# Optimization experiments

Measured on AMD Instinct MI355X. Metric: run time of the kernel, lower is better.

## Reference

```python
import jax, jax.numpy as jnp
import numpy as np
from jax import lax

NUM_BLOCKS = 3
NUM_LAYERS = 10
NL = NUM_BLOCKS * NUM_LAYERS  # 30 res blocks
RC = 512   # residual channels
GC = 512   # gate channels
SC = 512   # skip channels
KS = 2     # kernel size
CIN = 128  # local-conditioning channels
FRONT = 32 # front conv kernel size
OUT = 2    # gaussian (mean, log_std)
UPS = [16, 16]  # upsample scales, product = 256 hop
SQRT_HALF = 0.7071067811865476


def causal_conv1d(x, w, b, dilation):
    # x: [B,C_in,T], w: [C_out,C_in,K] -> left-pad only == torch pad-both + trim right (causal SAME)
    pad = dilation * (w.shape[-1] - 1)
    y = lax.conv_general_dilated(x, w, window_strides=(1,), padding=[(pad, 0)],
                                 rhs_dilation=(dilation,),
                                 dimension_numbers=('NCH', 'OIH', 'NCH'))
    return y + b[None, :, None]


def pw(x, w, b):
    # 1x1 conv: w [C_out,C_in]
    return jnp.einsum('oi,bit->bot', w, x) + b[None, :, None]


def upsample(c, up_w, up_b):
    # c: [B,CIN,Tm]; torch ConvTranspose2d(1,1,(3,2s),pad=(1,s//2),stride=(1,s)) + LeakyReLU(0.4)
    h = c[:, None]  # [B,1,CIN,Tm]
    for j, s in enumerate(UPS):
        k = up_w[j][:, :, ::-1, ::-1]  # flip kernel: transposed conv as lhs-dilated conv
        pw_ = 2 * s - 1 - s // 2       # = K - 1 - torch_pad along width
        h = lax.conv_general_dilated(h, k, window_strides=(1, 1),
                                     padding=[(1, 1), (pw_, pw_)],
                                     lhs_dilation=(1, s),
                                     dimension_numbers=('NCHW', 'OIHW', 'NCHW')) + up_b[j]
        h = jnp.where(h > 0, h, 0.4 * h)  # LeakyReLU(0.4)
    return h[:, 0]  # [B,CIN,T]


def setup_inputs() -> dict:
    key = jax.random.key(0)
    ks = iter(jax.random.split(key, 32))
    def rn(shape, scale):
        return jax.random.normal(next(ks), shape, dtype=jnp.float32) * scale
    B, T_mel = 1, 16
    T = T_mel * 256
    return {
        'x': rn((B, 1, T), 1.0),
        'c': rn((B, CIN, T_mel), 1.0),
        'front_w': rn((RC, 1, FRONT), 0.2),
        'front_b': rn((RC,), 0.05),
        'filt_w': rn((NL, GC, RC, KS), 0.03),
        'filt_b': rn((NL, GC), 0.05),
        'gate_w': rn((NL, GC, RC, KS), 0.03),
        'gate_b': rn((NL, GC), 0.05),
        'cf_w': rn((NL, GC, CIN), 0.05),
        'cf_b': rn((NL, GC), 0.05),
        'cg_w': rn((NL, GC, CIN), 0.05),
        'cg_b': rn((NL, GC), 0.05),
        'res_w': rn((NL, RC, GC), 0.04),
        'res_b': rn((NL, RC), 0.05),
        'skip_w': rn((NL, SC, GC), 0.04),
        'skip_b': rn((NL, SC), 0.05),
        'fin1_w': rn((SC, SC), 0.04),
        'fin1_b': rn((SC,), 0.05),
        'fin2_w': rn((OUT, SC), 0.04),
        'fin2_b': rn((OUT,), 0.05),
        'up_w': rn((2, 1, 1, 3, 2 * 16), 0.1),
        'up_b': rn((2,), 0.05),
    }


def reference(x, c, front_w, front_b, filt_w, filt_b, gate_w, gate_b,
              cf_w, cf_b, cg_w, cg_b, res_w, res_b, skip_w, skip_b,
              fin1_w, fin1_b, fin2_w, fin2_b, up_w, up_b):
    c_up = upsample(c, up_w, up_b)                       # [B,CIN,T]
    h = jax.nn.relu(causal_conv1d(x, front_w, front_b, 1))  # [B,RC,T]
    skip = jnp.zeros((x.shape[0], SC, x.shape[2]), x.dtype)
    for i in range(NL):
        d = KS ** (i % NUM_LAYERS)
        f = causal_conv1d(h, filt_w[i], filt_b[i], d) + pw(c_up, cf_w[i], cf_b[i])
        g = causal_conv1d(h, gate_w[i], gate_b[i], d) + pw(c_up, cg_w[i], cg_b[i])
        o = jnp.tanh(f) * jax.nn.sigmoid(g)
        h = (h + pw(o, res_w[i], res_b[i])) * SQRT_HALF
        skip = skip + pw(o, skip_w[i], skip_b[i])
    out = jax.nn.relu(skip)
    out = jax.nn.relu(pw(out, fin1_w, fin1_b))
    return pw(out, fin2_w, fin2_b)  # [B,OUT,T]
```

## Files before the change

### kernel.cpp

```cpp
#include <hip/hip_runtime.h>
#include <hip/hip_bf16.h>

#define TLEN 4096
#define HPADT 512
#define SQRT_HALF 0.70710678118654752f

typedef __attribute__((ext_vector_type(8))) short short8;
typedef __attribute__((ext_vector_type(4))) float floatx4;
typedef __attribute__((ext_vector_type(4))) unsigned short ushort4v;

#define MFMA_BF16(a, b, c) __builtin_amdgcn_mfma_f32_16x16x32_bf16((a), (b), (c), 0, 0, 0)

__device__ __forceinline__ float bf2f(unsigned short u) {
  union { unsigned int i; float f; } v; v.i = ((unsigned int)u) << 16; return v.f;
}
__device__ __forceinline__ unsigned short f2bf(float x) {
  union { float f; unsigned int i; } v; v.f = x;
  unsigned int r = v.i + 0x7FFFu + ((v.i >> 16) & 1u);
  return (unsigned short)(r >> 16);
}
__device__ __forceinline__ short8 ld8(const unsigned short* p) { return *(const short8*)p; }

template <int NI>
__device__ __forceinline__ void stage128(unsigned short* lds, const unsigned short* src,
                                         int stride, int tid) {
  #pragma unroll
  for (int inst = 0; inst < NI; ++inst) {
    int qb = inst * 256 + (tid & 192);
    int q = qb + (tid & 63);
    int r = q >> 4;
    int c = (q & 15) ^ (r & 15);
    __builtin_amdgcn_global_load_lds(
        (const __attribute__((address_space(1))) unsigned int*)(src + (size_t)r * stride + (c << 3)),
        (__attribute__((address_space(3))) unsigned int*)(lds + qb * 8),
        16, 0, 0);
  }
}
__device__ __forceinline__ short8 frag128(const unsigned short* lds, int r, int cj) {
  return *(const short8*)(lds + r * 128 + ((cj ^ (r & 15)) << 3));
}

template <int NI>
__device__ __forceinline__ void stage64(unsigned short* lds, const unsigned short* src,
                                        int stride, int tid) {
  #pragma unroll
  for (int inst = 0; inst < NI; ++inst) {
    int qb = inst * 256 + (tid & 192);
    int q = qb + (tid & 63);
    int r = q >> 3;
    int c = (q & 7) ^ (r & 7);
    __builtin_amdgcn_global_load_lds(
        (const __attribute__((address_space(1))) unsigned int*)(src + (size_t)r * stride + (c << 3)),
        (__attribute__((address_space(3))) unsigned int*)(lds + qb * 8),
        16, 0, 0);
  }
}
__device__ __forceinline__ short8 frag64(const unsigned short* lds, int r, int cj) {
  return *(const short8*)(lds + r * 64 + ((cj ^ (r & 7)) << 3));
}

__device__ __forceinline__ void wait_vm12() { asm volatile("s_waitcnt vmcnt(12)" ::: "memory"); }
__device__ __forceinline__ void wait_vm6()  { asm volatile("s_waitcnt vmcnt(6)"  ::: "memory"); }
__device__ __forceinline__ void wait_vm0()  { asm volatile("s_waitcnt vmcnt(0)"  ::: "memory"); }

__global__ __launch_bounds__(256) void cast_wa_kernel(
    const float* __restrict__ fw, const float* __restrict__ gw,
    unsigned short* __restrict__ WA, int base, int count)
{
  for (int i = blockIdx.x * 256 + threadIdx.x; i < count; i += gridDim.x * 256) {
    size_t idx = (size_t)base + i;
    size_t l = idx >> 16;
    int o = (int)((idx >> 7) & 511);
    int i4 = (int)(idx & 127) * 4;
    const float4* fp = (const float4*)(fw + (((l * 512 + o) * 512 + i4) * 2));
    const float4* gp = (const float4*)(gw + (((l * 512 + o) * 512 + i4) * 2));
    float4 f0 = fp[0], f1v = fp[1];
    float4 g0 = gp[0], g1 = gp[1];
    size_t base0 = ((l * 2 + 0) * 1024);
    size_t base1 = ((l * 2 + 1) * 1024);
    *(ushort4v*)&WA[(base0 + o) * 512 + i4]       = (ushort4v){f2bf(f0.x), f2bf(f0.z), f2bf(f1v.x), f2bf(f1v.z)};
    *(ushort4v*)&WA[(base1 + o) * 512 + i4]       = (ushort4v){f2bf(f0.y), f2bf(f0.w), f2bf(f1v.y), f2bf(f1v.w)};
    *(ushort4v*)&WA[(base0 + 512 + o) * 512 + i4] = (ushort4v){f2bf(g0.x), f2bf(g0.z), f2bf(g1.x), f2bf(g1.z)};
    *(ushort4v*)&WA[(base1 + 512 + o) * 512 + i4] = (ushort4v){f2bf(g0.y), f2bf(g0.w), f2bf(g1.y), f2bf(g1.w)};
  }
}

__global__ __launch_bounds__(256) void cast_rs_kernel(
    const float* __restrict__ rw, const float* __restrict__ sw,
    unsigned short* __restrict__ RS, int base, int count)
{
  for (int i = blockIdx.x * 256 + threadIdx.x; i < count; i += gridDim.x * 256) {
    size_t idx = (size_t)base + i;
    size_t l = idx >> 16;
    int o = (int)((idx >> 7) & 511);
    int i4 = (int)(idx & 127) * 4;
    float4 r4 = *(const float4*)(rw + ((l * 512 + o) * 512 + i4));
    float4 s4 = *(const float4*)(sw + ((l * 512 + o) * 512 + i4));
    *(ushort4v*)&RS[(l * 1024 + o) * 512 + i4]       = (ushort4v){f2bf(r4.x), f2bf(r4.y), f2bf(r4.z), f2bf(r4.w)};
    *(ushort4v*)&RS[(l * 1024 + 512 + o) * 512 + i4] = (ushort4v){f2bf(s4.x), f2bf(s4.y), f2bf(s4.z), f2bf(s4.w)};
  }
}

__global__ __launch_bounds__(256) void cast_misc_kernel(
    const float* __restrict__ cf, const float* __restrict__ cg,
    const float* __restrict__ f1, const float* __restrict__ fb,
    const float* __restrict__ cfb, const float* __restrict__ gb,
    const float* __restrict__ cgb,
    unsigned short* __restrict__ CA, unsigned short* __restrict__ F1c,
    float* __restrict__ fgb)
{
  const int total = 491520 + 65536 + 30720;
  for (int i = blockIdx.x * 256 + threadIdx.x; i < total; i += gridDim.x * 256) {
    if (i < 491520) {
      size_t idx = i;
      size_t l = idx >> 14;
      int o = (int)((idx >> 5) & 511);
      int i4 = (int)(idx & 31) * 4;
      float4 f4 = *(const float4*)(cf + ((l * 512 + o) * 128 + i4));
      float4 g4 = *(const float4*)(cg + ((l * 512 + o) * 128 + i4));
      *(ushort4v*)&CA[(l * 1024 + o) * 128 + i4]       = (ushort4v){f2bf(f4.x), f2bf(f4.y), f2bf(f4.z), f2bf(f4.w)};
      *(ushort4v*)&CA[(l * 1024 + 512 + o) * 128 + i4] = (ushort4v){f2bf(g4.x), f2bf(g4.y), f2bf(g4.z), f2bf(g4.w)};
    } else if (i < 491520 + 65536) {
      size_t idx = i - 491520;
      float4 v = *(const float4*)(f1 + idx * 4);
      *(ushort4v*)&F1c[idx * 4] = (ushort4v){f2bf(v.x), f2bf(v.y), f2bf(v.z), f2bf(v.w)};
    } else {
      int idx = i - (491520 + 65536);
      int l = idx >> 10, r = idx & 1023;
      float v;
      if (r < 512) v = fb[l * 512 + r] + cfb[l * 512 + r];
      else         v = gb[l * 512 + r - 512] + cgb[l * 512 + r - 512];
      fgb[idx] = v;
    }
  }
}


__global__ __launch_bounds__(256) void upsample1_kernel(
    const float* __restrict__ c, const float* __restrict__ up_w,
    const float* __restrict__ up_b, float* __restrict__ u1)
{
  int x = threadIdx.x;
  int h = blockIdx.x;
  const float* w = up_w;
  float acc = 0.f;
  int k1 = (23 - x) & 15;
  #pragma unroll
  for (int dk = 0; dk < 2; ++dk) {
    int kx = k1 + 16 * dk;
    int num = x + kx - 23;
    if (num >= 0) {
      int qq = num >> 4;
      if (qq < 16) {
        #pragma unroll
        for (int ky = 0; ky < 3; ++ky) {
          int hh = h + ky - 1;
          if (hh >= 0 && hh < 128)
            acc += c[hh * 16 + qq] * w[(2 - ky) * 32 + (31 - kx)];
        }
      }
    }
  }
  acc += up_b[0];
  u1[h * 256 + x] = acc > 0.f ? acc : 0.4f * acc;
}

__global__ __launch_bounds__(256) void upsample2_kernel(
    const float* __restrict__ u1, const float* __restrict__ up_w,
    const float* __restrict__ up_b, unsigned short* __restrict__ cu)
{
  int x = blockIdx.x * 256 + threadIdx.x;
  int h = blockIdx.y;
  const float* w = up_w + 96;
  float acc = 0.f;
  int k1 = (23 - x) & 15;
  #pragma unroll
  for (int dk = 0; dk < 2; ++dk) {
    int kx = k1 + 16 * dk;
    int num = x + kx - 23;
    if (num >= 0) {
      int qq = num >> 4;
      if (qq < 256) {
        #pragma unroll
        for (int ky = 0; ky < 3; ++ky) {
          int hh = h + ky - 1;
          if (hh >= 0 && hh < 128)
            acc += u1[hh * 256 + qq] * w[(2 - ky) * 32 + (31 - kx)];
        }
      }
    }
  }
  acc += up_b[1];
  acc = acc > 0.f ? acc : 0.4f * acc;
  cu[(size_t)x * 128 + h] = f2bf(acc);
}

__global__ __launch_bounds__(256) void front_kernel(
    const float* __restrict__ x, const float* __restrict__ fw, const float* __restrict__ fb,
    float* __restrict__ hf, unsigned short* __restrict__ hbf)
{
  __shared__ float xs[40];
  int tid = threadIdx.x;
  int o = blockIdx.y * 256 + tid;
  int t0 = blockIdx.x * 8;
  if (tid < 39) {
    int gx = t0 - 31 + tid;
    xs[tid] = (gx >= 0) ? x[gx] : 0.f;
  }
  __syncthreads();
  float w[32];
  #pragma unroll
  for (int k = 0; k < 32; ++k) w[k] = fw[o * 32 + k];
  float b = fb[o];
  #pragma unroll
  for (int j = 0; j < 8; ++j) {
    float acc = b;
    #pragma unroll
    for (int k = 0; k < 32; ++k) acc += w[k] * xs[j + k];
    acc = acc > 0.f ? acc : 0.f;
    int t = t0 + j;
    hf[(size_t)t * 512 + o] = acc;
    hbf[(size_t)(HPADT + t) * 512 + o] = f2bf(acc);
  }
}

template <int XU>
__global__ __launch_bounds__(256, 2) void gemm_a_smalld_kernel(
    const unsigned short* __restrict__ WA,
    const unsigned short* __restrict__ CA,
    const float* __restrict__ fgb,
    const unsigned short* __restrict__ hbf,
    const unsigned short* __restrict__ cu,
    unsigned short* __restrict__ obf,
    const int d)
{
  __shared__ unsigned short U[2][XU * 32 * 64];
  __shared__ unsigned short Aw[2][4][32 * 64];

  const int tid = threadIdx.x;
  const int lane = tid & 63;
  const int wave = tid >> 6;
  const int lm = lane & 15, qd = lane >> 4;
  const int n0 = blockIdx.x * 128;
  const int m0 = blockIdx.y * 32;
  const int wn = wave * 32;
  const int NS = 10;

  floatx4 accF[2][2], accG[2][2];
  #pragma unroll
  for (int a = 0; a < 2; ++a)
    #pragma unroll
    for (int b = 0; b < 2; ++b) {
      accF[a][b] = (floatx4){0.f, 0.f, 0.f, 0.f};
      accG[a][b] = (floatx4){0.f, 0.f, 0.f, 0.f};
    }

  auto stage_step = [&](int s, int b) {
    if (s < 8) {
      int k0 = s * 64;
      stage64<XU>(&U[b][0], hbf + (size_t)(HPADT + n0 - d) * 512 + k0, 512, tid);
      stage64<1>(&Aw[b][0][0], WA + (size_t)m0 * 512 + k0, 512, tid);
      stage64<1>(&Aw[b][1][0], WA + 524288 + (size_t)m0 * 512 + k0, 512, tid);
      stage64<1>(&Aw[b][2][0], WA + (size_t)(512 + m0) * 512 + k0, 512, tid);
      stage64<1>(&Aw[b][3][0], WA + 524288 + (size_t)(512 + m0) * 512 + k0, 512, tid);
    } else {
      int k0 = (s - 8) * 64;
      stage64<4>(&U[b][0], cu + (size_t)n0 * 128 + k0, 128, tid);
      stage64<1>(&Aw[b][0][0], CA + (size_t)m0 * 128 + k0, 128, tid);
      stage64<1>(&Aw[b][2][0], CA + (size_t)(512 + m0) * 128 + k0, 128, tid);
    }
  };

  stage_step(0, 0);
  #pragma unroll 1
  for (int s = 0; s < NS; ++s) {
    __syncthreads();
    if (s + 1 < NS) stage_step(s + 1, (s + 1) & 1);
    const unsigned short* u   = &U[s & 1][0];
    const unsigned short* af0 = &Aw[s & 1][0][0];
    const unsigned short* af1 = &Aw[s & 1][1][0];
    const unsigned short* ag0 = &Aw[s & 1][2][0];
    const unsigned short* ag1 = &Aw[s & 1][3][0];
    if (s < 8) {
      #pragma unroll
      for (int j = 0; j < 2; ++j) {
        int cj = j * 4 + qd;
        short8 f0a = frag64(af0, lm, cj),      f0b = frag64(af0, 16 + lm, cj);
        short8 f1a = frag64(af1, lm, cj),      f1b = frag64(af1, 16 + lm, cj);
        short8 g0a = frag64(ag0, lm, cj),      g0b = frag64(ag0, 16 + lm, cj);
        short8 g1a = frag64(ag1, lm, cj),      g1b = frag64(ag1, 16 + lm, cj);
        short8 x0 = frag64(u, wn + lm, cj);
        short8 x1 = frag64(u, wn + 16 + lm, cj);
        short8 y0 = frag64(u, d + wn + lm, cj);
        short8 y1 = frag64(u, d + wn + 16 + lm, cj);
        accF[0][0] = MFMA_BF16(f0a, x0, accF[0][0]);
        accF[0][0] = MFMA_BF16(f1a, y0, accF[0][0]);
        accF[0][1] = MFMA_BF16(f0a, x1, accF[0][1]);
        accF[0][1] = MFMA_BF16(f1a, y1, accF[0][1]);
        accF[1][0] = MFMA_BF16(f0b, x0, accF[1][0]);
        accF[1][0] = MFMA_BF16(f1b, y0, accF[1][0]);
        accF[1][1] = MFMA_BF16(f0b, x1, accF[1][1]);
        accF[1][1] = MFMA_BF16(f1b, y1, accF[1][1]);
        accG[0][0] = MFMA_BF16(g0a, x0, accG[0][0]);
        accG[0][0] = MFMA_BF16(g1a, y0, accG[0][0]);
        accG[0][1] = MFMA_BF16(g0a, x1, accG[0][1]);
        accG[0][1] = MFMA_BF16(g1a, y1, accG[0][1]);
        accG[1][0] = MFMA_BF16(g0b, x0, accG[1][0]);
        accG[1][0] = MFMA_BF16(g1b, y0, accG[1][0]);
        accG[1][1] = MFMA_BF16(g0b, x1, accG[1][1]);
        accG[1][1] = MFMA_BF16(g1b, y1, accG[1][1]);
      }
    } else {
      #pragma unroll
      for (int j = 0; j < 2; ++j) {
        int cj = j * 4 + qd;
        short8 fa = frag64(af0, lm, cj), fbv = frag64(af0, 16 + lm, cj);
        short8 ga = frag64(ag0, lm, cj), gbv = frag64(ag0, 16 + lm, cj);
        short8 x0 = frag64(u, wn + lm, cj);
        short8 x1 = frag64(u, wn + 16 + lm, cj);
        accF[0][0] = MFMA_BF16(fa, x0, accF[0][0]);
        accF[0][1] = MFMA_BF16(fa, x1, accF[0][1]);
        accF[1][0] = MFMA_BF16(fbv, x0, accF[1][0]);
        accF[1][1] = MFMA_BF16(fbv, x1, accF[1][1]);
        accG[0][0] = MFMA_BF16(ga, x0, accG[0][0]);
        accG[0][1] = MFMA_BF16(ga, x1, accG[0][1]);
        accG[1][0] = MFMA_BF16(gbv, x0, accG[1][0]);
        accG[1][1] = MFMA_BF16(gbv, x1, accG[1][1]);
      }
    }
  }

  #pragma unroll
  for (int mt = 0; mt < 2; ++mt) {
    int oc0 = m0 + mt * 16 + qd * 4;
    floatx4 fb4 = *(const floatx4*)&fgb[oc0];
    floatx4 gb4 = *(const floatx4*)&fgb[512 + oc0];
    #pragma unroll
    for (int nt = 0; nt < 2; ++nt) {
      int t = n0 + wn + nt * 16 + lm;
      ushort4v o4;
      #pragma unroll
      for (int r = 0; r < 4; ++r) {
        float f = accF[mt][nt][r] + fb4[r];
        float g = accG[mt][nt][r] + gb4[r];
        float ef = __expf(-2.f * f);
        float th = (1.f - ef) / (1.f + ef);
        float sg = 1.f / (1.f + __expf(-g));
        o4[r] = f2bf(th * sg);
      }
      *(ushort4v*)&obf[(size_t)t * 512 + oc0] = o4;
    }
  }
}

__global__ __launch_bounds__(256, 2) void gemm_a_kernel(
    const unsigned short* __restrict__ WA,
    const unsigned short* __restrict__ CA,
    const float* __restrict__ fgb,
    const unsigned short* __restrict__ hbf,
    const unsigned short* __restrict__ cu,
    unsigned short* __restrict__ obf,
    const int d)
{
  __shared__ unsigned short Af[3][32 * 64];
  __shared__ unsigned short Ag[3][32 * 64];
  __shared__ unsigned short Xs[3][128 * 64];

  const int tid = threadIdx.x;
  const int lane = tid & 63;
  const int wave = tid >> 6;
  const int lm = lane & 15, qd = lane >> 4;
  const int n0 = blockIdx.x * 128;
  const int m0 = blockIdx.y * 32;
  const int wn = wave * 32;
  const int NS = 18;

  floatx4 accF[2][2], accG[2][2];
  #pragma unroll
  for (int a = 0; a < 2; ++a)
    #pragma unroll
    for (int b = 0; b < 2; ++b) {
      accF[a][b] = (floatx4){0.f, 0.f, 0.f, 0.f};
      accG[a][b] = (floatx4){0.f, 0.f, 0.f, 0.f};
    }

  auto stage_step = [&](int s, int b) {
    if (s < 16) {
      int tap = s >> 3;
      int k0 = (s & 7) * 64;
      const unsigned short* ab = WA + (size_t)tap * 524288;
      stage64<1>(&Af[b][0], ab + (size_t)m0 * 512 + k0, 512, tid);
      stage64<1>(&Ag[b][0], ab + (size_t)(512 + m0) * 512 + k0, 512, tid);
      stage64<4>(&Xs[b][0], hbf + (size_t)(HPADT + n0 - (tap ? 0 : d)) * 512 + k0, 512, tid);
    } else {
      int k0 = (s - 16) * 64;
      stage64<1>(&Af[b][0], CA + (size_t)m0 * 128 + k0, 128, tid);
      stage64<1>(&Ag[b][0], CA + (size_t)(512 + m0) * 128 + k0, 128, tid);
      stage64<4>(&Xs[b][0], cu + (size_t)n0 * 128 + k0, 128, tid);
    }
  };

  stage_step(0, 0);
  stage_step(1, 1);
  int cur = 0;
  #pragma unroll 1
  for (int s = 0; s < NS; ++s) {
    int stg = cur + 2; if (stg >= 3) stg -= 3;
    if (s + 2 < NS) stage_step(s + 2, stg);
    if (s + 2 < NS)      wait_vm12();
    else if (s + 1 < NS) wait_vm6();
    else                 wait_vm0();
    __builtin_amdgcn_s_barrier();
    __builtin_amdgcn_sched_barrier(0);
    const unsigned short* af = &Af[cur][0];
    const unsigned short* ag = &Ag[cur][0];
    const unsigned short* xs = &Xs[cur][0];
    __builtin_amdgcn_s_setprio(1);
    #pragma unroll
    for (int j = 0; j < 2; ++j) {
      int cj = j * 4 + qd;
      short8 a0 = frag64(af, lm, cj);
      short8 a1 = frag64(af, 16 + lm, cj);
      short8 g0 = frag64(ag, lm, cj);
      short8 g1 = frag64(ag, 16 + lm, cj);
      short8 x0 = frag64(xs, wn + lm, cj);
      short8 x1 = frag64(xs, wn + 16 + lm, cj);
      accF[0][0] = MFMA_BF16(a0, x0, accF[0][0]);
      accF[0][1] = MFMA_BF16(a0, x1, accF[0][1]);
      accF[1][0] = MFMA_BF16(a1, x0, accF[1][0]);
      accF[1][1] = MFMA_BF16(a1, x1, accF[1][1]);
      accG[0][0] = MFMA_BF16(g0, x0, accG[0][0]);
      accG[0][1] = MFMA_BF16(g0, x1, accG[0][1]);
      accG[1][0] = MFMA_BF16(g1, x0, accG[1][0]);
      accG[1][1] = MFMA_BF16(g1, x1, accG[1][1]);
    }
    __builtin_amdgcn_s_setprio(0);
    __builtin_amdgcn_sched_barrier(0);
    __builtin_amdgcn_s_barrier();
    __builtin_amdgcn_sched_barrier(0);
    cur = (cur == 2) ? 0 : cur + 1;
  }

  #pragma unroll
  for (int mt = 0; mt < 2; ++mt) {
    int oc0 = m0 + mt * 16 + qd * 4;
    floatx4 fb4 = *(const floatx4*)&fgb[oc0];
    floatx4 gb4 = *(const floatx4*)&fgb[512 + oc0];
    #pragma unroll
    for (int nt = 0; nt < 2; ++nt) {
      int t = n0 + wn + nt * 16 + lm;
      ushort4v o4;
      #pragma unroll
      for (int r = 0; r < 4; ++r) {
        float f = accF[mt][nt][r] + fb4[r];
        float g = accG[mt][nt][r] + gb4[r];
        float ef = __expf(-2.f * f);
        float th = (1.f - ef) / (1.f + ef);
        float sg = 1.f / (1.f + __expf(-g));
        o4[r] = f2bf(th * sg);
      }
      *(ushort4v*)&obf[(size_t)t * 512 + oc0] = o4;
    }
  }
}

__global__ __launch_bounds__(256, 2) void gemm_b_kernel(
    const unsigned short* __restrict__ RS,
    const float* __restrict__ rb, const float* __restrict__ sb,
    const unsigned short* __restrict__ obf,
    float* __restrict__ hf, unsigned short* __restrict__ hbf,
    float* __restrict__ skip, unsigned short* __restrict__ skipbf,
    const int first, const int last)
{
  __shared__ unsigned short Ar[3][32 * 64];
  __shared__ unsigned short As_[3][32 * 64];
  __shared__ unsigned short Xs[3][128 * 64];

  const int tid = threadIdx.x;
  const int lane = tid & 63;
  const int wave = tid >> 6;
  const int lm = lane & 15, qd = lane >> 4;
  const int n0 = blockIdx.x * 128;
  const int m0 = blockIdx.y * 32;
  const int wn = wave * 32;
  const int NS = 8;

  floatx4 accR[2][2], accS[2][2];
  #pragma unroll
  for (int a = 0; a < 2; ++a)
    #pragma unroll
    for (int b = 0; b < 2; ++b) {
      accR[a][b] = (floatx4){0.f, 0.f, 0.f, 0.f};
      accS[a][b] = (floatx4){0.f, 0.f, 0.f, 0.f};
    }

  auto stage_step = [&](int s, int b) {
    int k0 = s * 64;
    stage64<1>(&Ar[b][0], RS + (size_t)m0 * 512 + k0, 512, tid);
    stage64<1>(&As_[b][0], RS + (size_t)(512 + m0) * 512 + k0, 512, tid);
    stage64<4>(&Xs[b][0], obf + (size_t)n0 * 512 + k0, 512, tid);
  };

  stage_step(0, 0);
  stage_step(1, 1);
  int cur = 0;
  #pragma unroll 1
  for (int s = 0; s < NS; ++s) {
    int stg = cur + 2; if (stg >= 3) stg -= 3;
    if (s + 2 < NS) stage_step(s + 2, stg);
    if (s + 2 < NS)      wait_vm12();
    else if (s + 1 < NS) wait_vm6();
    else                 wait_vm0();
    __builtin_amdgcn_s_barrier();
    __builtin_amdgcn_sched_barrier(0);
    const unsigned short* ar = &Ar[cur][0];
    const unsigned short* as = &As_[cur][0];
    const unsigned short* xs = &Xs[cur][0];
    __builtin_amdgcn_s_setprio(1);
    #pragma unroll
    for (int j = 0; j < 2; ++j) {
      int cj = j * 4 + qd;
      short8 a0 = frag64(ar, lm, cj);
      short8 a1 = frag64(ar, 16 + lm, cj);
      short8 g0 = frag64(as, lm, cj);
      short8 g1 = frag64(as, 16 + lm, cj);
      short8 x0 = frag64(xs, wn + lm, cj);
      short8 x1 = frag64(xs, wn + 16 + lm, cj);
      accR[0][0] = MFMA_BF16(a0, x0, accR[0][0]);
      accR[0][1] = MFMA_BF16(a0, x1, accR[0][1]);
      accR[1][0] = MFMA_BF16(a1, x0, accR[1][0]);
      accR[1][1] = MFMA_BF16(a1, x1, accR[1][1]);
      accS[0][0] = MFMA_BF16(g0, x0, accS[0][0]);
      accS[0][1] = MFMA_BF16(g0, x1, accS[0][1]);
      accS[1][0] = MFMA_BF16(g1, x0, accS[1][0]);
      accS[1][1] = MFMA_BF16(g1, x1, accS[1][1]);
    }
    __builtin_amdgcn_s_setprio(0);
    __builtin_amdgcn_sched_barrier(0);
    __builtin_amdgcn_s_barrier();
    __builtin_amdgcn_sched_barrier(0);
    cur = (cur == 2) ? 0 : cur + 1;
  }

  #pragma unroll
  for (int mt = 0; mt < 2; ++mt) {
    int oc0 = m0 + mt * 16 + qd * 4;
    floatx4 rb4 = *(const floatx4*)&rb[oc0];
    floatx4 sb4 = *(const floatx4*)&sb[oc0];
    #pragma unroll
    for (int nt = 0; nt < 2; ++nt) {
      int t = n0 + wn + nt * 16 + lm;
      size_t base = (size_t)t * 512 + oc0;
      floatx4 h4 = *(const floatx4*)&hf[base];
      floatx4 s4;
      if (first) s4 = (floatx4){0.f, 0.f, 0.f, 0.f};
      else s4 = *(const floatx4*)&skip[base];
      ushort4v hb4;
      #pragma unroll
      for (int r = 0; r < 4; ++r) {
        float hv = (h4[r] + accR[mt][nt][r] + rb4[r]) * SQRT_HALF;
        h4[r] = hv;
        hb4[r] = f2bf(hv);
        s4[r] = s4[r] + accS[mt][nt][r] + sb4[r];
      }
      *(floatx4*)&hf[base] = h4;
      *(ushort4v*)&hbf[(size_t)(HPADT + t) * 512 + oc0] = hb4;
      *(floatx4*)&skip[base] = s4;
      if (last) {
        ushort4v sk4;
        #pragma unroll
        for (int r = 0; r < 4; ++r) sk4[r] = f2bf(s4[r] > 0.f ? s4[r] : 0.f);
        *(ushort4v*)&skipbf[base] = sk4;
      }
    }
  }
}

__global__ __launch_bounds__(256) void final1_kernel(
    const unsigned short* __restrict__ W1,
    const float* __restrict__ b1,
    const unsigned short* __restrict__ skipbf,
    unsigned short* __restrict__ t1)
{
  __shared__ unsigned short Aw[2][64 * 128];
  __shared__ unsigned short Xs[2][128 * 128];

  const int tid = threadIdx.x;
  const int lane = tid & 63;
  const int wave = tid >> 6;
  const int lm = lane & 15, qd = lane >> 4;
  const int n0 = blockIdx.x * 128;
  const int m0 = blockIdx.y * 64;
  const int wm = (wave & 1) * 32;
  const int wn = (wave >> 1) * 64;

  floatx4 acc[2][4];
  #pragma unroll
  for (int a = 0; a < 2; ++a)
    #pragma unroll
    for (int b = 0; b < 4; ++b) acc[a][b] = (floatx4){0.f, 0.f, 0.f, 0.f};

  auto stage_step = [&](int s, int b) {
    int k0 = s * 128;
    stage128<4>(&Aw[b][0], W1 + (size_t)m0 * 512 + k0, 512, tid);
    stage128<8>(&Xs[b][0], skipbf + (size_t)n0 * 512 + k0, 512, tid);
  };

  stage_step(0, 0);
  for (int s = 0; s < 4; ++s) {
    __syncthreads();
    if (s < 3) stage_step(s + 1, (s + 1) & 1);
    const unsigned short* aw = &Aw[s & 1][0];
    const unsigned short* xs = &Xs[s & 1][0];
    #pragma unroll
    for (int j = 0; j < 4; ++j) {
      int cj = j * 4 + qd;
      short8 a[2], xv[4];
      a[0] = frag128(aw, wm + lm, cj);
      a[1] = frag128(aw, wm + 16 + lm, cj);
      #pragma unroll
      for (int nt = 0; nt < 4; ++nt) xv[nt] = frag128(xs, wn + nt * 16 + lm, cj);
      #pragma unroll
      for (int mt = 0; mt < 2; ++mt)
        #pragma unroll
        for (int nt = 0; nt < 4; ++nt)
          acc[mt][nt] = MFMA_BF16(a[mt], xv[nt], acc[mt][nt]);
    }
  }

  #pragma unroll
  for (int mt = 0; mt < 2; ++mt) {
    int oc0 = m0 + wm + mt * 16 + qd * 4;
    floatx4 b4 = *(const floatx4*)&b1[oc0];
    #pragma unroll
    for (int nt = 0; nt < 4; ++nt) {
      int t = n0 + wn + nt * 16 + lm;
      ushort4v o4;
      #pragma unroll
      for (int r = 0; r < 4; ++r) {
        float v = acc[mt][nt][r] + b4[r];
        o4[r] = f2bf(v > 0.f ? v : 0.f);
      }
      *(ushort4v*)&t1[(size_t)t * 512 + oc0] = o4;
    }
  }
}

__global__ __launch_bounds__(256) void final2_kernel(
    const float* __restrict__ W2, const float* __restrict__ b2,
    const unsigned short* __restrict__ t1, float* __restrict__ out)
{
  int wave = threadIdx.x >> 6, lane = threadIdx.x & 63;
  int t = blockIdx.x * 4 + wave;
  short8 v = ld8(t1 + (size_t)t * 512 + lane * 8);
  float a0 = 0.f, a1 = 0.f;
  #pragma unroll
  for (int r = 0; r < 8; ++r) {
    float f = bf2f((unsigned short)v[r]);
    a0 += W2[lane * 8 + r] * f;
    a1 += W2[512 + lane * 8 + r] * f;
  }
  #pragma unroll
  for (int off = 32; off > 0; off >>= 1) {
    a0 += __shfl_xor(a0, off, 64);
    a1 += __shfl_xor(a1, off, 64);
  }
  if (lane == 0) {
    out[t] = a0 + b2[0];
    out[TLEN + t] = a1 + b2[1];
  }
}

extern "C" void kernel_launch(void* const* d_in, const int* in_sizes, int n_in,
                              void* d_out, int out_size, void* d_ws, size_t ws_size,
                              hipStream_t stream) {
  (void)in_sizes; (void)n_in; (void)out_size; (void)ws_size;
  const float* x       = (const float*)d_in[0];
  const float* c       = (const float*)d_in[1];
  const float* front_w = (const float*)d_in[2];
  const float* front_b = (const float*)d_in[3];
  const float* filt_w  = (const float*)d_in[4];
  const float* filt_b  = (const float*)d_in[5];
  const float* gate_w  = (const float*)d_in[6];
  const float* gate_b  = (const float*)d_in[7];
  const float* cf_w    = (const float*)d_in[8];
  const float* cf_b    = (const float*)d_in[9];
  const float* cg_w    = (const float*)d_in[10];
  const float* cg_b    = (const float*)d_in[11];
  const float* res_w   = (const float*)d_in[12];
  const float* res_b   = (const float*)d_in[13];
  const float* skip_w  = (const float*)d_in[14];
  const float* skip_b  = (const float*)d_in[15];
  const float* fin1_w  = (const float*)d_in[16];
  const float* fin1_b  = (const float*)d_in[17];
  const float* fin2_w  = (const float*)d_in[18];
  const float* fin2_b  = (const float*)d_in[19];
  const float* up_w    = (const float*)d_in[20];
  const float* up_b    = (const float*)d_in[21];

  char* ws = (char*)d_ws;
  auto alloc = [&](size_t bytes) {
    char* p = ws;
    ws += (bytes + 255) & ~(size_t)255;
    return p;
  };
  unsigned short* WA     = (unsigned short*)alloc((size_t)30 * 2 * 1024 * 512 * 2);
  unsigned short* RS     = (unsigned short*)alloc((size_t)30 * 1024 * 512 * 2);
  unsigned short* CA     = (unsigned short*)alloc((size_t)30 * 1024 * 128 * 2);
  unsigned short* F1c    = (unsigned short*)alloc((size_t)512 * 512 * 2);
  float* fgb             = (float*)alloc((size_t)30 * 1024 * 4);
  float* u1              = (float*)alloc((size_t)128 * 256 * 4);
  unsigned short* cu     = (unsigned short*)alloc((size_t)TLEN * 128 * 2);
  float* hf              = (float*)alloc((size_t)TLEN * 512 * 4);
  unsigned short* hbf    = (unsigned short*)alloc((size_t)(HPADT + TLEN + 256) * 512 * 2);
  unsigned short* obf    = (unsigned short*)alloc((size_t)TLEN * 512 * 2);
  float* skip            = (float*)alloc((size_t)TLEN * 512 * 4);
  unsigned short* skipbf = (unsigned short*)alloc((size_t)TLEN * 512 * 2);
  unsigned short* t1     = (unsigned short*)alloc((size_t)TLEN * 512 * 2);
  float* out             = (float*)d_out;

  hipMemsetAsync(hbf, 0, (size_t)HPADT * 512 * 2, stream);

  for (int g = 0; g < 6; ++g)
    cast_wa_kernel<<<512, 256, 0, stream>>>(filt_w, gate_w, WA, g * 327680, 327680);
  for (int g = 0; g < 6; ++g)
    cast_rs_kernel<<<512, 256, 0, stream>>>(res_w, skip_w, RS, g * 327680, 327680);
  cast_misc_kernel<<<512, 256, 0, stream>>>(cf_w, cg_w, fin1_w, filt_b, cf_b,
                                            gate_b, cg_b, CA, F1c, fgb);

  upsample1_kernel<<<dim3(128), 256, 0, stream>>>(c, up_w, up_b, u1);
  upsample2_kernel<<<dim3(16, 128), 256, 0, stream>>>(u1, up_w, up_b, cu);
  front_kernel<<<dim3(512, 2), 256, 0, stream>>>(x, front_w, front_b, hf, hbf);

  for (int l = 0; l < 30; ++l) {
    int d = 1 << (l % 10);
    if (d <= 32) {
      gemm_a_smalld_kernel<5><<<dim3(32, 16), 256, 0, stream>>>(
          WA + (size_t)l * 2 * 524288, CA + (size_t)l * 131072,
          fgb + (size_t)l * 1024, hbf, cu, obf, d);
    } else if (d == 64) {
      gemm_a_smalld_kernel<6><<<dim3(32, 16), 256, 0, stream>>>(
          WA + (size_t)l * 2 * 524288, CA + (size_t)l * 131072,
          fgb + (size_t)l * 1024, hbf, cu, obf, d);
    } else {
      gemm_a_kernel<<<dim3(32, 16), 256, 0, stream>>>(
          WA + (size_t)l * 2 * 524288, CA + (size_t)l * 131072,
          fgb + (size_t)l * 1024, hbf, cu, obf, d);
    }
    gemm_b_kernel<<<dim3(32, 16), 256, 0, stream>>>(
        RS + (size_t)l * 524288,
        res_b + (size_t)l * 512, skip_b + (size_t)l * 512,
        obf, hf, hbf, skip, skipbf, (l == 0) ? 1 : 0, (l == 29) ? 1 : 0);
  }

  final1_kernel<<<dim3(32, 8), 256, 0, stream>>>(F1c, fin1_b, skipbf, t1);
  final2_kernel<<<1024, 256, 0, stream>>>(fin2_w, fin2_b, t1, out);
}
```

Before: 1.281 ms.

## Use 512-thread blocks with 256-wide time tiles and merged weight staging

The three per-layer GEMM kernels now run 8 waves per block over 256 time steps instead of 4 waves over 128, so each staged weight tile is shared by twice as many columns. Filter and gate weight tiles are loaded together into one LDS buffer by a single staging call. The pipeline goes from triple to double buffering, and the small-dilation kernel drops __syncthreads for explicit vmcnt waits plus barriers. This halves the grid to 256 blocks, which may underfill the GPU, and the hbf padding is enlarged to cover the wider tile's halo reads.

```diff
diff --git a/kernel.cpp b/kernel.cpp
--- a/kernel.cpp
+++ b/kernel.cpp
@@ -41,11 +41,11 @@
 }
 
 template <int NI>
-__device__ __forceinline__ void stage64(unsigned short* lds, const unsigned short* src,
-                                        int stride, int tid) {
+__device__ __forceinline__ void stage64w8(unsigned short* lds, const unsigned short* src,
+                                          int stride, int tid) {
   #pragma unroll
   for (int inst = 0; inst < NI; ++inst) {
-    int qb = inst * 256 + (tid & 192);
+    int qb = inst * 512 + (tid & 448);
     int q = qb + (tid & 63);
     int r = q >> 3;
     int c = (q & 7) ^ (r & 7);
@@ -55,13 +55,26 @@
         16, 0, 0);
   }
 }
+__device__ __forceinline__ void stageA(unsigned short* lds, const unsigned short* f,
+                                       const unsigned short* g, int strideA, int tid) {
+  int qb = (tid & 448);
+  int q = qb + (tid & 63);
+  int r = q >> 3;
+  int c = (q & 7) ^ (r & 7);
+  const unsigned short* src =
+      (r < 32 ? f + (size_t)r * strideA : g + (size_t)(r - 32) * strideA) + (c << 3);
+  __builtin_amdgcn_global_load_lds(
+      (const __attribute__((address_space(1))) unsigned int*)src,
+      (__attribute__((address_space(3))) unsigned int*)(lds + qb * 8),
+      16, 0, 0);
+}
 __device__ __forceinline__ short8 frag64(const unsigned short* lds, int r, int cj) {
   return *(const short8*)(lds + r * 64 + ((cj ^ (r & 7)) << 3));
 }
 
-__device__ __forceinline__ void wait_vm12() { asm volatile("s_waitcnt vmcnt(12)" ::: "memory"); }
-__device__ __forceinline__ void wait_vm6()  { asm volatile("s_waitcnt vmcnt(6)"  ::: "memory"); }
-__device__ __forceinline__ void wait_vm0()  { asm volatile("s_waitcnt vmcnt(0)"  ::: "memory"); }
+__device__ __forceinline__ void wait_vm7() { asm volatile("s_waitcnt vmcnt(7)" ::: "memory"); }
+__device__ __forceinline__ void wait_vm5() { asm volatile("s_waitcnt vmcnt(5)" ::: "memory"); }
+__device__ __forceinline__ void wait_vm0() { asm volatile("s_waitcnt vmcnt(0)" ::: "memory"); }
 
 __global__ __launch_bounds__(256) void cast_wa_kernel(
     const float* __restrict__ fw, const float* __restrict__ gw,
@@ -224,8 +237,7 @@
   }
 }
 
-template <int XU>
-__global__ __launch_bounds__(256, 2) void gemm_a_smalld_kernel(
+__global__ __launch_bounds__(512, 2) void gemm_a_smalld_kernel(
     const unsigned short* __restrict__ WA,
     const unsigned short* __restrict__ CA,
     const float* __restrict__ fgb,
@@ -234,14 +246,14 @@
     unsigned short* __restrict__ obf,
     const int d)
 {
-  __shared__ unsigned short U[2][XU * 32 * 64];
-  __shared__ unsigned short Aw[2][4][32 * 64];
+  __shared__ unsigned short U[2][320 * 64];
+  __shared__ unsigned short Aw[2][128 * 64];
 
   const int tid = threadIdx.x;
   const int lane = tid & 63;
   const int wave = tid >> 6;
   const int lm = lane & 15, qd = lane >> 4;
-  const int n0 = blockIdx.x * 128;
+  const int n0 = blockIdx.x * 256;
   const int m0 = blockIdx.y * 32;
   const int wn = wave * 32;
   const int NS = 10;
@@ -258,76 +270,83 @@
   auto stage_step = [&](int s, int b) {
     if (s < 8) {
       int k0 = s * 64;
-      stage64<XU>(&U[b][0], hbf + (size_t)(HPADT + n0 - d) * 512 + k0, 512, tid);
-      stage64<1>(&Aw[b][0][0], WA + (size_t)m0 * 512 + k0, 512, tid);
-      stage64<1>(&Aw[b][1][0], WA + 524288 + (size_t)m0 * 512 + k0, 512, tid);
-      stage64<1>(&Aw[b][2][0], WA + (size_t)(512 + m0) * 512 + k0, 512, tid);
-      stage64<1>(&Aw[b][3][0], WA + 524288 + (size_t)(512 + m0) * 512 + k0, 512, tid);
+      stage64w8<5>(&U[b][0], hbf + (size_t)(HPADT + n0 - d) * 512 + k0, 512, tid);
+      stageA(&Aw[b][0],       WA + (size_t)m0 * 512 + k0,
+                              WA + (size_t)(512 + m0) * 512 + k0, 512, tid);
+      stageA(&Aw[b][64 * 64], WA + 524288 + (size_t)m0 * 512 + k0,
+                              WA + 524288 + (size_t)(512 + m0) * 512 + k0, 512, tid);
     } else {
       int k0 = (s - 8) * 64;
-      stage64<4>(&U[b][0], cu + (size_t)n0 * 128 + k0, 128, tid);
-      stage64<1>(&Aw[b][0][0], CA + (size_t)m0 * 128 + k0, 128, tid);
-      stage64<1>(&Aw[b][2][0], CA + (size_t)(512 + m0) * 128 + k0, 128, tid);
+      stage64w8<4>(&U[b][0], cu + (size_t)n0 * 128 + k0, 128, tid);
+      stageA(&Aw[b][0], CA + (size_t)m0 * 128 + k0,
+                        CA + (size_t)(512 + m0) * 128 + k0, 128, tid);
     }
   };
 
   stage_step(0, 0);
   #pragma unroll 1
   for (int s = 0; s < NS; ++s) {
-    __syncthreads();
     if (s + 1 < NS) stage_step(s + 1, (s + 1) & 1);
-    const unsigned short* u   = &U[s & 1][0];
-    const unsigned short* af0 = &Aw[s & 1][0][0];
-    const unsigned short* af1 = &Aw[s & 1][1][0];
-    const unsigned short* ag0 = &Aw[s & 1][2][0];
-    const unsigned short* ag1 = &Aw[s & 1][3][0];
+    if (s + 1 < 8)        wait_vm7();
+    else if (s + 1 < NS)  wait_vm5();
+    else                  wait_vm0();
+    __builtin_amdgcn_s_barrier();
+    __builtin_amdgcn_sched_barrier(0);
+    const unsigned short* u  = &U[s & 1][0];
+    const unsigned short* aw = &Aw[s & 1][0];
+    __builtin_amdgcn_s_setprio(1);
     if (s < 8) {
       #pragma unroll
       for (int j = 0; j < 2; ++j) {
         int cj = j * 4 + qd;
-        short8 f0a = frag64(af0, lm, cj),      f0b = frag64(af0, 16 + lm, cj);
-        short8 f1a = frag64(af1, lm, cj),      f1b = frag64(af1, 16 + lm, cj);
-        short8 g0a = frag64(ag0, lm, cj),      g0b = frag64(ag0, 16 + lm, cj);
-        short8 g1a = frag64(ag1, lm, cj),      g1b = frag64(ag1, 16 + lm, cj);
-        short8 x0 = frag64(u, wn + lm, cj);
-        short8 x1 = frag64(u, wn + 16 + lm, cj);
-        short8 y0 = frag64(u, d + wn + lm, cj);
-        short8 y1 = frag64(u, d + wn + 16 + lm, cj);
-        accF[0][0] = MFMA_BF16(f0a, x0, accF[0][0]);
-        accF[0][0] = MFMA_BF16(f1a, y0, accF[0][0]);
-        accF[0][1] = MFMA_BF16(f0a, x1, accF[0][1]);
-        accF[0][1] = MFMA_BF16(f1a, y1, accF[0][1]);
-        accF[1][0] = MFMA_BF16(f0b, x0, accF[1][0]);
-        accF[1][0] = MFMA_BF16(f1b, y0, accF[1][0]);
-        accF[1][1] = MFMA_BF16(f0b, x1, accF[1][1]);
-        accF[1][1] = MFMA_BF16(f1b, y1, accF[1][1]);
-        accG[0][0] = MFMA_BF16(g0a, x0, accG[0][0]);
-        accG[0][0] = MFMA_BF16(g1a, y0, accG[0][0]);
-        accG[0][1] = MFMA_BF16(g0a, x1, accG[0][1]);
-        accG[0][1] = MFMA_BF16(g1a, y1, accG[0][1]);
-        accG[1][0] = MFMA_BF16(g0b, x0, accG[1][0]);
-        accG[1][0] = MFMA_BF16(g1b, y0, accG[1][0]);
-        accG[1][1] = MFMA_BF16(g0b, x1, accG[1][1]);
-        accG[1][1] = MFMA_BF16(g1b, y1, accG[1][1]);
+        short8 f0[2], g0[2], f1[2], g1[2], xv[2], yv[2];
+        #pragma unroll
+        for (int mt = 0; mt < 2; ++mt) {
+          f0[mt] = frag64(aw, mt * 16 + lm, cj);
+          g0[mt] = frag64(aw, 32 + mt * 16 + lm, cj);
+          f1[mt] = frag64(aw, 64 + mt * 16 + lm, cj);
+          g1[mt] = frag64(aw, 96 + mt * 16 + lm, cj);
+        }
+        #pragma unroll
+        for (int nt = 0; nt < 2; ++nt) {
+          xv[nt] = frag64(u, wn + nt * 16 + lm, cj);
+          yv[nt] = frag64(u, d + wn + nt * 16 + lm, cj);
+        }
+        #pragma unroll
+        for (int mt = 0; mt < 2; ++mt)
+          #pragma unroll
+          for (int nt = 0; nt < 2; ++nt) {
+            accF[mt][nt] = MFMA_BF16(f0[mt], xv[nt], accF[mt][nt]);
+            accF[mt][nt] = MFMA_BF16(f1[mt], yv[nt], accF[mt][nt]);
+            accG[mt][nt] = MFMA_BF16(g0[mt], xv[nt], accG[mt][nt]);
+            accG[mt][nt] = MFMA_BF16(g1[mt], yv[nt], accG[mt][nt]);
+          }
       }
     } else {
       #pragma unroll
       for (int j = 0; j < 2; ++j) {
         int cj = j * 4 + qd;
-        short8 fa = frag64(af0, lm, cj), fbv = frag64(af0, 16 + lm, cj);
-        short8 ga = frag64(ag0, lm, cj), gbv = frag64(ag0, 16 + lm, cj);
-        short8 x0 = frag64(u, wn + lm, cj);
-        short8 x1 = frag64(u, wn + 16 + lm, cj);
-        accF[0][0] = MFMA_BF16(fa, x0, accF[0][0]);
-        accF[0][1] = MFMA_BF16(fa, x1, accF[0][1]);
-        accF[1][0] = MFMA_BF16(fbv, x0, accF[1][0]);
-        accF[1][1] = MFMA_BF16(fbv, x1, accF[1][1]);
-        accG[0][0] = MFMA_BF16(ga, x0, accG[0][0]);
-        accG[0][1] = MFMA_BF16(ga, x1, accG[0][1]);
-        accG[1][0] = MFMA_BF16(gbv, x0, accG[1][0]);
-        accG[1][1] = MFMA_BF16(gbv, x1, accG[1][1]);
-      }
-    }
+        short8 fv[2], gv[2], xv[2];
+        #pragma unroll
+        for (int mt = 0; mt < 2; ++mt) {
+          fv[mt] = frag64(aw, mt * 16 + lm, cj);
+          gv[mt] = frag64(aw, 32 + mt * 16 + lm, cj);
+        }
+        #pragma unroll
+        for (int nt = 0; nt < 2; ++nt) xv[nt] = frag64(u, wn + nt * 16 + lm, cj);
+        #pragma unroll
+        for (int mt = 0; mt < 2; ++mt)
+          #pragma unroll
+          for (int nt = 0; nt < 2; ++nt) {
+            accF[mt][nt] = MFMA_BF16(fv[mt], xv[nt], accF[mt][nt]);
+            accG[mt][nt] = MFMA_BF16(gv[mt], xv[nt], accG[mt][nt]);
+          }
+      }
+    }
+    __builtin_amdgcn_s_setprio(0);
+    __builtin_amdgcn_sched_barrier(0);
+    __builtin_amdgcn_s_barrier();
+    __builtin_amdgcn_sched_barrier(0);
   }
 
   #pragma unroll
@@ -353,7 +372,7 @@
   }
 }
 
-__global__ __launch_bounds__(256, 2) void gemm_a_kernel(
+__global__ __launch_bounds__(512, 2) void gemm_a_bigd_kernel(
     const unsigned short* __restrict__ WA,
     const unsigned short* __restrict__ CA,
     const float* __restrict__ fgb,
@@ -362,15 +381,14 @@
     unsigned short* __restrict__ obf,
     const int d)
 {
-  __shared__ unsigned short Af[3][32 * 64];
-  __shared__ unsigned short Ag[3][32 * 64];
-  __shared__ unsigned short Xs[3][128 * 64];
+  __shared__ unsigned short U[2][256 * 64];
+  __shared__ unsigned short Aw[2][64 * 64];
 
   const int tid = threadIdx.x;
   const int lane = tid & 63;
   const int wave = tid >> 6;
   const int lm = lane & 15, qd = lane >> 4;
-  const int n0 = blockIdx.x * 128;
+  const int n0 = blockIdx.x * 256;
   const int m0 = blockIdx.y * 32;
   const int wn = wave * 32;
   const int NS = 18;
@@ -388,57 +406,51 @@
     if (s < 16) {
       int tap = s >> 3;
       int k0 = (s & 7) * 64;
-      const unsigned short* ab = WA + (size_t)tap * 524288;
-      stage64<1>(&Af[b][0], ab + (size_t)m0 * 512 + k0, 512, tid);
-      stage64<1>(&Ag[b][0], ab + (size_t)(512 + m0) * 512 + k0, 512, tid);
-      stage64<4>(&Xs[b][0], hbf + (size_t)(HPADT + n0 - (tap ? 0 : d)) * 512 + k0, 512, tid);
+      stage64w8<4>(&U[b][0], hbf + (size_t)(HPADT + n0 - (tap ? 0 : d)) * 512 + k0, 512, tid);
+      stageA(&Aw[b][0], WA + (size_t)tap * 524288 + (size_t)m0 * 512 + k0,
+                        WA + (size_t)tap * 524288 + (size_t)(512 + m0) * 512 + k0, 512, tid);
     } else {
       int k0 = (s - 16) * 64;
-      stage64<1>(&Af[b][0], CA + (size_t)m0 * 128 + k0, 128, tid);
-      stage64<1>(&Ag[b][0], CA + (size_t)(512 + m0) * 128 + k0, 128, tid);
-      stage64<4>(&Xs[b][0], cu + (size_t)n0 * 128 + k0, 128, tid);
+      stage64w8<4>(&U[b][0], cu + (size_t)n0 * 128 + k0, 128, tid);
+      stageA(&Aw[b][0], CA + (size_t)m0 * 128 + k0,
+                        CA + (size_t)(512 + m0) * 128 + k0, 128, tid);
     }
   };
 
   stage_step(0, 0);
-  stage_step(1, 1);
-  int cur = 0;
   #pragma unroll 1
   for (int s = 0; s < NS; ++s) {
-    int stg = cur + 2; if (stg >= 3) stg -= 3;
-    if (s + 2 < NS) stage_step(s + 2, stg);
-    if (s + 2 < NS)      wait_vm12();
-    else if (s + 1 < NS) wait_vm6();
-    else                 wait_vm0();
+    if (s + 1 < NS) stage_step(s + 1, (s + 1) & 1);
+    if (s + 1 < NS) wait_vm5();
+    else            wait_vm0();
     __builtin_amdgcn_s_barrier();
     __builtin_amdgcn_sched_barrier(0);
-    const unsigned short* af = &Af[cur][0];
-    const unsigned short* ag = &Ag[cur][0];
-    const unsigned short* xs = &Xs[cur][0];
+    const unsigned short* u  = &U[s & 1][0];
+    const unsigned short* aw = &Aw[s & 1][0];
     __builtin_amdgcn_s_setprio(1);
     #pragma unroll
     for (int j = 0; j < 2; ++j) {
       int cj = j * 4 + qd;
-      short8 a0 = frag64(af, lm, cj);
-      short8 a1 = frag64(af, 16 + lm, cj);
-      short8 g0 = frag64(ag, lm, cj);
-      short8 g1 = frag64(ag, 16 + lm, cj);
-      short8 x0 = frag64(xs, wn + lm, cj);
-      short8 x1 = frag64(xs, wn + 16 + lm, cj);
-      accF[0][0] = MFMA_BF16(a0, x0, accF[0][0]);
-      accF[0][1] = MFMA_BF16(a0, x1, accF[0][1]);
-      accF[1][0] = MFMA_BF16(a1, x0, accF[1][0]);
-      accF[1][1] = MFMA_BF16(a1, x1, accF[1][1]);
-      accG[0][0] = MFMA_BF16(g0, x0, accG[0][0]);
-      accG[0][1] = MFMA_BF16(g0, x1, accG[0][1]);
-      accG[1][0] = MFMA_BF16(g1, x0, accG[1][0]);
-      accG[1][1] = MFMA_BF16(g1, x1, accG[1][1]);
+      short8 fv[2], gv[2], xv[2];
+      #pragma unroll
+      for (int mt = 0; mt < 2; ++mt) {
+        fv[mt] = frag64(aw, mt * 16 + lm, cj);
+        gv[mt] = frag64(aw, 32 + mt * 16 + lm, cj);
+      }
+      #pragma unroll
+      for (int nt = 0; nt < 2; ++nt) xv[nt] = frag64(u, wn + nt * 16 + lm, cj);
+      #pragma unroll
+      for (int mt = 0; mt < 2; ++mt)
+        #pragma unroll
+        for (int nt = 0; nt < 2; ++nt) {
+          accF[mt][nt] = MFMA_BF16(fv[mt], xv[nt], accF[mt][nt]);
+          accG[mt][nt] = MFMA_BF16(gv[mt], xv[nt], accG[mt][nt]);
+        }
     }
     __builtin_amdgcn_s_setprio(0);
     __builtin_amdgcn_sched_barrier(0);
     __builtin_amdgcn_s_barrier();
     __builtin_amdgcn_sched_barrier(0);
-    cur = (cur == 2) ? 0 : cur + 1;
   }
 
   #pragma unroll
@@ -464,7 +476,7 @@
   }
 }
 
-__global__ __launch_bounds__(256, 2) void gemm_b_kernel(
+__global__ __launch_bounds__(512, 2) void gemm_b_kernel(
     const unsigned short* __restrict__ RS,
     const float* __restrict__ rb, const float* __restrict__ sb,
     const unsigned short* __restrict__ obf,
@@ -472,15 +484,14 @@
     float* __restrict__ skip, unsigned short* __restrict__ skipbf,
     const int first, const int last)
 {
-  __shared__ unsigned short Ar[3][32 * 64];
-  __shared__ unsigned short As_[3][32 * 64];
-  __shared__ unsigned short Xs[3][128 * 64];
+  __shared__ unsigned short U[2][256 * 64];
+  __shared__ unsigned short Aw[2][64 * 64];
 
   const int tid = threadIdx.x;
   const int lane = tid & 63;
   const int wave = tid >> 6;
   const int lm = lane & 15, qd = lane >> 4;
-  const int n0 = blockIdx.x * 128;
+  const int n0 = blockIdx.x * 256;
   const int m0 = blockIdx.y * 32;
   const int wn = wave * 32;
   const int NS = 8;
@@ -496,50 +507,45 @@
 
   auto stage_step = [&](int s, int b) {
     int k0 = s * 64;
-    stage64<1>(&Ar[b][0], RS + (size_t)m0 * 512 + k0, 512, tid);
-    stage64<1>(&As_[b][0], RS + (size_t)(512 + m0) * 512 + k0, 512, tid);
-    stage64<4>(&Xs[b][0], obf + (size_t)n0 * 512 + k0, 512, tid);
+    stage64w8<4>(&U[b][0], obf + (size_t)n0 * 512 + k0, 512, tid);
+    stageA(&Aw[b][0], RS + (size_t)m0 * 512 + k0,
+                      RS + (size_t)(512 + m0) * 512 + k0, 512, tid);
   };
 
   stage_step(0, 0);
-  stage_step(1, 1);
-  int cur = 0;
   #pragma unroll 1
   for (int s = 0; s < NS; ++s) {
-    int stg = cur + 2; if (stg >= 3) stg -= 3;
-    if (s + 2 < NS) stage_step(s + 2, stg);
-    if (s + 2 < NS)      wait_vm12();
-    else if (s + 1 < NS) wait_vm6();
-    else                 wait_vm0();
+    if (s + 1 < NS) stage_step(s + 1, (s + 1) & 1);
+    if (s + 1 < NS) wait_vm5();
+    else            wait_vm0();
     __builtin_amdgcn_s_barrier();
     __builtin_amdgcn_sched_barrier(0);
-    const unsigned short* ar = &Ar[cur][0];
-    const unsigned short* as = &As_[cur][0];
-    const unsigned short* xs = &Xs[cur][0];
+    const unsigned short* u  = &U[s & 1][0];
+    const unsigned short* aw = &Aw[s & 1][0];
     __builtin_amdgcn_s_setprio(1);
     #pragma unroll
     for (int j = 0; j < 2; ++j) {
       int cj = j * 4 + qd;
-      short8 a0 = frag64(ar, lm, cj);
-      short8 a1 = frag64(ar, 16 + lm, cj);
-      short8 g0 = frag64(as, lm, cj);
-      short8 g1 = frag64(as, 16 + lm, cj);
-      short8 x0 = frag64(xs, wn + lm, cj);
-      short8 x1 = frag64(xs, wn + 16 + lm, cj);
-      accR[0][0] = MFMA_BF16(a0, x0, accR[0][0]);
-      accR[0][1] = MFMA_BF16(a0, x1, accR[0][1]);
-      accR[1][0] = MFMA_BF16(a1, x0, accR[1][0]);
-      accR[1][1] = MFMA_BF16(a1, x1, accR[1][1]);
-      accS[0][0] = MFMA_BF16(g0, x0, accS[0][0]);
-      accS[0][1] = MFMA_BF16(g0, x1, accS[0][1]);
-      accS[1][0] = MFMA_BF16(g1, x0, accS[1][0]);
-      accS[1][1] = MFMA_BF16(g1, x1, accS[1][1]);
+      short8 rv[2], sv[2], xv[2];
+      #pragma unroll
+      for (int mt = 0; mt < 2; ++mt) {
+        rv[mt] = frag64(aw, mt * 16 + lm, cj);
+        sv[mt] = frag64(aw, 32 + mt * 16 + lm, cj);
+      }
+      #pragma unroll
+      for (int nt = 0; nt < 2; ++nt) xv[nt] = frag64(u, wn + nt * 16 + lm, cj);
+      #pragma unroll
+      for (int mt = 0; mt < 2; ++mt)
+        #pragma unroll
+        for (int nt = 0; nt < 2; ++nt) {
+          accR[mt][nt] = MFMA_BF16(rv[mt], xv[nt], accR[mt][nt]);
+          accS[mt][nt] = MFMA_BF16(sv[mt], xv[nt], accS[mt][nt]);
+        }
     }
     __builtin_amdgcn_s_setprio(0);
     __builtin_amdgcn_sched_barrier(0);
     __builtin_amdgcn_s_barrier();
     __builtin_amdgcn_sched_barrier(0);
-    cur = (cur == 2) ? 0 : cur + 1;
   }
 
   #pragma unroll
@@ -712,7 +718,7 @@
   float* u1              = (float*)alloc((size_t)128 * 256 * 4);
   unsigned short* cu     = (unsigned short*)alloc((size_t)TLEN * 128 * 2);
   float* hf              = (float*)alloc((size_t)TLEN * 512 * 4);
-  unsigned short* hbf    = (unsigned short*)alloc((size_t)(HPADT + TLEN + 256) * 512 * 2);
+  unsigned short* hbf    = (unsigned short*)alloc((size_t)(HPADT + TLEN + 384) * 512 * 2);
   unsigned short* obf    = (unsigned short*)alloc((size_t)TLEN * 512 * 2);
   float* skip            = (float*)alloc((size_t)TLEN * 512 * 4);
   unsigned short* skipbf = (unsigned short*)alloc((size_t)TLEN * 512 * 2);
@@ -734,20 +740,16 @@
 
   for (int l = 0; l < 30; ++l) {
     int d = 1 << (l % 10);
-    if (d <= 32) {
-      gemm_a_smalld_kernel<5><<<dim3(32, 16), 256, 0, stream>>>(
-          WA + (size_t)l * 2 * 524288, CA + (size_t)l * 131072,
-          fgb + (size_t)l * 1024, hbf, cu, obf, d);
-    } else if (d == 64) {
-      gemm_a_smalld_kernel<6><<<dim3(32, 16), 256, 0, stream>>>(
+    if (d <= 64) {
+      gemm_a_smalld_kernel<<<dim3(16, 16), 512, 0, stream>>>(
           WA + (size_t)l * 2 * 524288, CA + (size_t)l * 131072,
           fgb + (size_t)l * 1024, hbf, cu, obf, d);
     } else {
-      gemm_a_kernel<<<dim3(32, 16), 256, 0, stream>>>(
+      gemm_a_bigd_kernel<<<dim3(16, 16), 512, 0, stream>>>(
           WA + (size_t)l * 2 * 524288, CA + (size_t)l * 131072,
           fgb + (size_t)l * 1024, hbf, cu, obf, d);
     }
-    gemm_b_kernel<<<dim3(32, 16), 256, 0, stream>>>(
+    gemm_b_kernel<<<dim3(16, 16), 512, 0, stream>>>(
         RS + (size_t)l * 524288,
         res_b + (size_t)l * 512, skip_b + (size_t)l * 512,
         obf, hf, hbf, skip, skipbf, (l == 0) ? 1 : 0, (l == 29) ? 1 : 0);
```

New measurement: 1.385 ms. 1.08x slower.
